# Optimization experiments

Hardware: AMD Instinct MI355X
Metric: run time of the kernel (lower is better)

The kernel has to match this reference:

```python
import jax, jax.numpy as jnp
import numpy as np

EOS = 1  # EOS_VALUE in the original code (word_label == 1 triggers end_sentence)
L_LAYERS = 2
B, T, H, E = 128, 256, 1024, 1024  # TD == E == input_size


def setup_inputs() -> dict:
    key = jax.random.key(0)
    ks = jax.random.split(key, 20)
    k = 1.0 / np.sqrt(H)
    u = lambda kk, shape: jax.random.uniform(kk, shape, jnp.float32, -k, k)
    inp = {
        "yy_pad": jax.random.randint(ks[0], (B, T), 0, E, dtype=jnp.int32),
        "h_t": jax.random.normal(ks[1], (L_LAYERS, B, H), jnp.float32),
        "h_t_rev": jax.random.normal(ks[2], (L_LAYERS, B, H), jnp.float32),
        "x_lens": jax.random.randint(ks[3], (B,), 1, T - 1, dtype=jnp.int32).at[0].set(T - 1),
        # parameters (layer 0 input size == E == H, so weights stack cleanly)
        "emb": jax.random.normal(ks[4], (E, E), jnp.float32) * 0.02,
        "W_ih": u(ks[5], (L_LAYERS, 4 * H, E)),
        "W_hh": u(ks[6], (L_LAYERS, 4 * H, H)),
        "b_ih": u(ks[7], (L_LAYERS, 4 * H)),
        "b_hh": u(ks[8], (L_LAYERS, 4 * H)),
        "W_ih_rev": u(ks[9], (L_LAYERS, 4 * H, E)),
        "W_hh_rev": u(ks[10], (L_LAYERS, 4 * H, H)),
        "b_ih_rev": u(ks[11], (L_LAYERS, 4 * H)),
        "b_hh_rev": u(ks[12], (L_LAYERS, 4 * H)),
        "c0": jnp.zeros((L_LAYERS, H), jnp.float32),
        "c0_rev": jnp.zeros((L_LAYERS, H), jnp.float32),
        "fc_W": u(ks[13], (E, 2 * H)),
        "fc_b": u(ks[14], (E,)),
    }
    return inp


def _lstm_cell(x, h, c, Wih, Whh, bih, bhh):
    # torch.nn.LSTMCell gate order: input, forget, cell(g), output
    z = x @ Wih.T + bih + h @ Whh.T + bhh  # [B, 4H]
    i, f, g, o = jnp.split(z, 4, axis=-1)
    c2 = jax.nn.sigmoid(f) * c + jax.nn.sigmoid(i) * jnp.tanh(g)
    h2 = jax.nn.sigmoid(o) * jnp.tanh(c2)
    return h2, c2


def reference(yy_pad, h_t, h_t_rev, x_lens, emb, W_ih, W_hh, b_ih, b_hh,
              W_ih_rev, W_hh_rev, b_ih_rev, b_hh_rev, c0, c0_rev, fc_W, fc_b):
    batch = yy_pad.shape[0]
    n_steps = yy_pad.shape[1]  # == max(x_lens) + 1 by construction (static)
    eos_onehot = jax.nn.one_hot(EOS, fc_W.shape[0], dtype=fc_W.dtype)  # [TD]

    c_init = jnp.broadcast_to(c0[:, None, :], (L_LAYERS, batch, c0.shape[1]))
    c_init_rev = jnp.broadcast_to(c0_rev[:, None, :], (L_LAYERS, batch, c0.shape[1]))

    def step(carry, _):
        feed, h, hr, c, cr, ended = carry
        x = emb[feed]   # [B, E]  (sos embedding / previous argmax token)
        xr = x
        hs, hrs, cs, crs = [], [], [], []
        for l in range(L_LAYERS):
            hn, cn = _lstm_cell(x, h[l], c[l], W_ih[l], W_hh[l], b_ih[l], b_hh[l])
            hrn, crn = _lstm_cell(xr, hr[l], cr[l], W_ih_rev[l], W_hh_rev[l], b_ih_rev[l], b_hh_rev[l])
            hs.append(hn); cs.append(cn); hrs.append(hrn); crs.append(crn)
            x, xr = hn, hrn
        h, hr = jnp.stack(hs), jnp.stack(hrs)
        c, cr = jnp.stack(cs), jnp.stack(crs)
        # faithful to torch: cat([B,H],[B,H]) -> [B,2H] -> permute(1,0) -> reshape(B,-1)
        wh = jnp.concatenate([h[-1], hr[-1]], axis=-1).T.reshape(batch, -1)
        logits = wh @ fc_W.T + fc_b  # [B, TD]
        logits = jnp.where(ended[:, None], eos_onehot, logits)
        label = jnp.argmax(logits, axis=1).astype(jnp.int32)
        ended = ended | (label == EOS)
        return (label, h, hr, c, cr, ended), logits

    carry0 = (yy_pad[:, 0], h_t, h_t_rev, c_init, c_init_rev,
              jnp.zeros((batch,), jnp.bool_))
    _, logits_seq = jax.lax.scan(step, carry0, None, length=n_steps)  # [T, B, TD]
    return jax.nn.softmax(jnp.transpose(logits_seq, (1, 0, 2)), axis=-1)  # [B, T, TD]
```

## Files before the change

kernel.cpp:

```cpp
#include <hip/hip_runtime.h>
#include <math.h>

#define NB 128
#define NT 256
#define NH 1024
#define NE 1024
#define G4 4096
#define EOSL 1

#define Z_OFF    ((size_t)0)
#define C_OFF    ((size_t)1048576)
#define HT_OFF   ((size_t)1572864)
#define FCZ_OFF  ((size_t)1835008)
#define BIAS_OFF ((size_t)2883584)
#define END_OFF  ((size_t)2899968)
#define XPH_OFF  ((size_t)2900096)
#define XPX_OFF  ((size_t)3424384)
#define WP_OFF   ((size_t)3555456)
#define TOTAL_MIN_F  ((size_t)3555456)
#define TOTAL_PACK_F ((size_t)37109888)

typedef __attribute__((ext_vector_type(8))) short s8v;
typedef __attribute__((ext_vector_type(4))) float f4v;

struct GMF {
  const float* W[16];
  const unsigned short* Bp[16];
  const unsigned short* Wp[2];
};

__device__ __forceinline__ void add4(float4& d, const float4 a) {
  d.x += a.x; d.y += a.y; d.z += a.z; d.w += a.w;
}
__device__ __forceinline__ float sigmoid_stable(float x) {
  if (x >= 0.f) return 1.f / (1.f + expf(-x));
  float ex = expf(x);
  return ex / (1.f + ex);
}
__device__ __forceinline__ unsigned short bf_rne(float x) {
  unsigned u = __float_as_uint(x);
  return (unsigned short)((u + 0x7FFFu + ((u >> 16) & 1u)) >> 16);
}
__device__ __forceinline__ void split_bf(float x, unsigned short& h, unsigned short& l) {
  unsigned u = __float_as_uint(x);
  unsigned hb = (u + 0x7FFFu + ((u >> 16) & 1u)) >> 16;
  h = (unsigned short)hb;
  float r = x - __uint_as_float(hb << 16);
  l = bf_rne(r);
}
__device__ __forceinline__ void cvt8(float4 a0, float4 a1, s8v& hi, s8v& lo)
{
  const float v[8] = {a0.x, a0.y, a0.z, a0.w, a1.x, a1.y, a1.z, a1.w};
  #pragma unroll
  for (int j = 0; j < 8; j++) {
    unsigned short h, l; split_bf(v[j], h, l);
    hi[j] = (short)h; lo[j] = (short)l;
  }
}


__global__ void k_init(const int* yy, const float* h_t, const float* h_tr,
                       const float* c0, const float* c0r,
                       const float* b_ih, const float* b_hh,
                       const float* b_ihr, const float* b_hhr,
                       const float* emb,
                       unsigned short* xph, unsigned short* xpx,
                       float* call, float* bias, int* ended)
{
  int idx = blockIdx.x * 256 + threadIdx.x;
  if (idx < 2 * 2048 * 128) {
    int dir = idx / (2048 * 128); int rem = idx % (2048 * 128);
    int row = rem >> 7, b = rem & 127;
    int l = row >> 10, n = row & 1023;
    const float* src = dir ? h_tr : h_t;
    float v = src[((size_t)l * 128 + b) * 1024 + n];
    unsigned short h, lo; split_bf(v, h, lo);
    size_t off = ((size_t)(dir * 64 + (row >> 5)) * 8 + (b >> 4)) * 1024
               + ((b & 15) + 16 * ((n >> 3) & 3)) * 8 + (n & 7);
    xph[off] = h; xph[off + 512] = lo;
  }
  if (idx < 4 * 1024 * 128) {
    int ld = idx / (1024 * 128); int l = ld >> 1, dir = ld & 1;
    int rem = idx % (1024 * 128); int n = rem >> 7;
    call[idx] = (dir ? c0r : c0)[l * 1024 + n];
  }
  if (idx < 4 * 4096) {
    int ld = idx / 4096; int l = ld >> 1, dir = ld & 1;
    int m = idx & 4095;
    bias[idx] = (dir ? b_ihr : b_ih)[l * 4096 + m] + (dir ? b_hhr : b_hh)[l * 4096 + m];
  }
  if (idx < 128 * 1024) {
    int b = idx >> 10, k = idx & 1023;
    int e = yy[b * NT];
    float v = emb[(size_t)e * 1024 + k];
    unsigned short h, lo; split_bf(v, h, lo);
    size_t off = ((size_t)(k >> 5) * 8 + (b >> 4)) * 1024
               + ((b & 15) + 16 * ((k >> 3) & 3)) * 8 + (k & 7);
    xpx[off] = h; xpx[off + 512] = lo;
  }
  if (idx < NB) ended[idx] = 0;
}

__global__ void k_packW(const float* W_ih, const float* W_hh,
                        const float* W_ihr, const float* W_hhr,
                        unsigned short* WP)
{
  int idx = blockIdx.x * 256 + threadIdx.x;
  int l = idx & 63;
  int frag = idx >> 6;
  int ktile = frag & 63;
  int mtile = (frag >> 6) & 255;
  int ld = frag >> 14;
  int layer = ld >> 1, dir = ld & 1;
  int m = mtile * 16 + (l & 15);
  int kg = ktile * 32 + (l >> 4) * 8;
  const float* base;
  if (kg < 1024) base = (dir ? W_ihr : W_ih) + ((size_t)layer * 4096 + m) * 1024 + kg;
  else           base = (dir ? W_hhr : W_hh) + ((size_t)layer * 4096 + m) * 1024 + (kg - 1024);
  float4 a0 = *(const float4*)base, a1 = *(const float4*)(base + 4);
  s8v hi, lo; cvt8(a0, a1, hi, lo);
  unsigned short* outp = WP + (size_t)frag * 1024 + l * 8;
  *(s8v*)outp = hi;
  *(s8v*)(outp + 512) = lo;
}

__device__ __forceinline__ void red_write(float* red, int slot, int l, const f4v (&acc)[2][8])
{
  #pragma unroll
  for (int mt = 0; mt < 2; mt++)
    #pragma unroll
    for (int bt = 0; bt < 8; bt++)
      *(f4v*)&red[(size_t)slot * 4096 + (mt * 8 + bt) * 256 + l * 4] = acc[mt][bt];
}
__device__ __forceinline__ void red_add(const float* red, int slot, int l, f4v (&acc)[2][8])
{
  #pragma unroll
  for (int mt = 0; mt < 2; mt++)
    #pragma unroll
    for (int bt = 0; bt < 8; bt++)
      acc[mt][bt] += *(const f4v*)&red[(size_t)slot * 4096 + (mt * 8 + bt) * 256 + l * 4];
}

template<int PACKED>
__global__ __launch_bounds__(512, 2) void k_gemm(GMF d, float* z)
{
  const int mb = blockIdx.x, dir = blockIdx.y;
  const int tid = threadIdx.x, l = tid & 63, w = tid >> 6;
  const int m0 = mb * 32;
  const int lr = l & 15, lk = l >> 4;
  __shared__ __align__(16) float red[4 * 4096];

  f4v acc[2][8];
  #pragma unroll
  for (int mt = 0; mt < 2; mt++)
    #pragma unroll
    for (int bt = 0; bt < 8; bt++)
      acc[mt][bt] = (f4v)(0.0f);

  const unsigned short* Bb = d.Bp[dir * 8 + w] + l * 8;

  if (PACKED) {
    const unsigned short* Wb = d.Wp[dir]
        + (((size_t)(mb * 2) * 64 + w * 8) << 10) + l * 8;
    s8v whc[2], wlc[2];
    #pragma unroll
    for (int mt = 0; mt < 2; mt++) {
      const unsigned short* p = Wb + ((size_t)(mt * 64) << 10);
      whc[mt] = *(const s8v*)p; wlc[mt] = *(const s8v*)(p + 512);
    }
    #pragma unroll 1
    for (int kk = 0; kk < 8; kk++) {
      s8v bh[8], bl[8];
      #pragma unroll
      for (int bt = 0; bt < 8; bt++) {
        const unsigned short* p = Bb + ((size_t)(kk * 8 + bt) << 10);
        bh[bt] = *(const s8v*)p; bl[bt] = *(const s8v*)(p + 512);
      }
      s8v whn[2], wln[2];
      if (kk < 7) {
        #pragma unroll
        for (int mt = 0; mt < 2; mt++) {
          const unsigned short* p = Wb + ((size_t)(mt * 64 + kk + 1) << 10);
          whn[mt] = *(const s8v*)p; wln[mt] = *(const s8v*)(p + 512);
        }
      }
      #pragma unroll
      for (int mt = 0; mt < 2; mt++)
        #pragma unroll
        for (int bt = 0; bt < 8; bt++) {
          acc[mt][bt] = __builtin_amdgcn_mfma_f32_16x16x32_bf16(whc[mt], bh[bt], acc[mt][bt], 0, 0, 0);
          acc[mt][bt] = __builtin_amdgcn_mfma_f32_16x16x32_bf16(whc[mt], bl[bt], acc[mt][bt], 0, 0, 0);
          acc[mt][bt] = __builtin_amdgcn_mfma_f32_16x16x32_bf16(wlc[mt], bh[bt], acc[mt][bt], 0, 0, 0);
        }
      if (kk < 7) {
        whc[0] = whn[0]; whc[1] = whn[1];
        wlc[0] = wln[0]; wlc[1] = wln[1];
      }
    }
  } else {
    const float* Wb = d.W[dir * 8 + w] + (size_t)(m0 + lr) * 1024 + lk * 8;
    float4 ac[2][2];
    #pragma unroll
    for (int mt = 0; mt < 2; mt++) {
      ac[mt][0] = *(const float4*)(Wb + (size_t)mt * 16384);
      ac[mt][1] = *(const float4*)(Wb + (size_t)mt * 16384 + 4);
    }
    #pragma unroll 1
    for (int kk = 0; kk < 8; kk++) {
      s8v bh[8], bl[8];
      #pragma unroll
      for (int bt = 0; bt < 8; bt++) {
        const unsigned short* p = Bb + ((size_t)(kk * 8 + bt) << 10);
        bh[bt] = *(const s8v*)p; bl[bt] = *(const s8v*)(p + 512);
      }
      float4 an[2][2];
      if (kk < 7) {
        #pragma unroll
        for (int mt = 0; mt < 2; mt++) {
          an[mt][0] = *(const float4*)(Wb + (size_t)mt * 16384 + (kk + 1) * 32);
          an[mt][1] = *(const float4*)(Wb + (size_t)mt * 16384 + (kk + 1) * 32 + 4);
        }
      }
      #pragma unroll
      for (int mt = 0; mt < 2; mt++) {
        s8v wh, wl;
        cvt8(ac[mt][0], ac[mt][1], wh, wl);
        #pragma unroll
        for (int bt = 0; bt < 8; bt++) {
          acc[mt][bt] = __builtin_amdgcn_mfma_f32_16x16x32_bf16(wh, bh[bt], acc[mt][bt], 0, 0, 0);
          acc[mt][bt] = __builtin_amdgcn_mfma_f32_16x16x32_bf16(wh, bl[bt], acc[mt][bt], 0, 0, 0);
          acc[mt][bt] = __builtin_amdgcn_mfma_f32_16x16x32_bf16(wl, bh[bt], acc[mt][bt], 0, 0, 0);
        }
      }
      if (kk < 7) {
        #pragma unroll
        for (int mt = 0; mt < 2; mt++) { ac[mt][0] = an[mt][0]; ac[mt][1] = an[mt][1]; }
      }
    }
  }

  if (w >= 4) red_write(red, w - 4, l, acc);
  __syncthreads();
  if (w < 4) red_add(red, w, l, acc);
  __syncthreads();
  if (w == 2 || w == 3) red_write(red, w - 2, l, acc);
  __syncthreads();
  if (w < 2) red_add(red, w, l, acc);
  __syncthreads();
  if (w < 2) red_write(red, w, l, acc);
  __syncthreads();
  float* zb = z + (size_t)dir * 4096 * 128;
  #pragma unroll
  for (int vi = 0; vi < 2; vi++) {
    int v = tid + vi * 512;
    f4v s = *(const f4v*)&red[(size_t)v * 4];
    s += *(const f4v*)&red[(size_t)4096 + (size_t)v * 4];
    int frag = v >> 6, lane = v & 63;
    int mt = frag >> 3, bt = frag & 7;
    int m = m0 + mt * 16 + (lane >> 4) * 4;
    int b = bt * 16 + (lane & 15);
    #pragma unroll
    for (int r = 0; r < 4; r++)
      zb[(size_t)(m + r) * 128 + b] = s[r];
  }
}

__global__ void k_gates(const float* z, const float* bias, float* c,
                        unsigned short* xph, int ktile0, float* hB)
{
  int t = threadIdx.x;
  int idx = blockIdx.x * 256 + t;
  int n = idx >> 5, cc = (idx & 31) << 2;
  int dir = blockIdx.y;
  float4 g[4];
  #pragma unroll
  for (int gg = 0; gg < 4; gg++) {
    int row = gg * 1024 + n;
    float4 s = *(const float4*)(z + ((size_t)dir * 4096 + row) * 128 + cc);
    float b = bias[dir * 4096 + row];
    s.x += b; s.y += b; s.z += b; s.w += b;
    g[gg] = s;
  }
  float* cp = c + ((size_t)dir * 1024 + n) * 128 + cc;
  float4 cold = *(float4*)cp;
  float4 cn, hn;
  cn.x = sigmoid_stable(g[1].x) * cold.x + sigmoid_stable(g[0].x) * tanhf(g[2].x);
  cn.y = sigmoid_stable(g[1].y) * cold.y + sigmoid_stable(g[0].y) * tanhf(g[2].y);
  cn.z = sigmoid_stable(g[1].z) * cold.z + sigmoid_stable(g[0].z) * tanhf(g[2].z);
  cn.w = sigmoid_stable(g[1].w) * cold.w + sigmoid_stable(g[0].w) * tanhf(g[2].w);
  hn.x = sigmoid_stable(g[3].x) * tanhf(cn.x);
  hn.y = sigmoid_stable(g[3].y) * tanhf(cn.y);
  hn.z = sigmoid_stable(g[3].z) * tanhf(cn.z);
  hn.w = sigmoid_stable(g[3].w) * tanhf(cn.w);
  *(float4*)cp = cn;
  size_t fo = ((size_t)(dir * 64 + ktile0 + (n >> 5)) * 8 + (cc >> 4)) * 1024
            + ((cc & 15) + 16 * ((n >> 3) & 3)) * 8 + (n & 7);
  const float* hv = &hn.x;
  #pragma unroll
  for (int j = 0; j < 4; j++) {
    unsigned short h, lo; split_bf(hv[j], h, lo);
    xph[fo + j * 8] = h;
    xph[fo + j * 8 + 512] = lo;
  }
  if (hB)
    *(float4*)(hB + (size_t)dir * (1024 * 128) + (size_t)n * 128 + cc) = hn;
}

__global__ __launch_bounds__(256) void k_fc(const float* Ht, const float* fc_W, float* fcz)
{
  int et = blockIdx.x, kp = blockIdx.y;
  int e0 = et * 64;
  int k00 = kp * 256;
  __shared__ __align__(16) float in_s[128][36];
  __shared__ __align__(16) float w_s[64][36];
  int t = threadIdx.x, e_sub = t & 7, bg = t >> 3, b0 = bg * 4;
  float acc[8][4] = {};
  for (int kc = 0; kc < 256; kc += 32) {
    #pragma unroll
    for (int i = 0; i < 4; i++) {
      int flat = t + 256 * i, r = flat >> 3, f4i = flat & 7;
      const float* row = Ht + (r >= 64 ? (size_t)NH * NB + (size_t)(r - 64) * 2048
                                       : (size_t)r * 2048);
      float4 v = *(const float4*)(row + k00 + kc + f4i * 4);
      int sw = (f4i ^ (r >> 2)) & 7;
      *(float4*)&in_s[r][sw * 4] = v;
    }
    #pragma unroll
    for (int i = 0; i < 2; i++) {
      int flat = t + 256 * i, r = flat >> 3, f4i = flat & 7;
      *(float4*)&w_s[r][f4i * 4] =
          *(const float4*)(fc_W + (size_t)(e0 + r) * 2048 + k00 + kc + f4i * 4);
    }
    __syncthreads();
    #pragma unroll
    for (int kq = 0; kq < 8; kq++) {
      int ksw = (kq ^ bg) & 7;
      float4 a4[4];
      #pragma unroll
      for (int ib = 0; ib < 4; ib++) a4[ib] = *(const float4*)&in_s[b0 + ib][ksw * 4];
      float4 w4[8];
      #pragma unroll
      for (int je = 0; je < 8; je++) w4[je] = *(const float4*)&w_s[e_sub + 8 * je][kq * 4];
      #pragma unroll
      for (int je = 0; je < 8; je++)
        #pragma unroll
        for (int ib = 0; ib < 4; ib++)
          acc[je][ib] += a4[ib].x * w4[je].x + a4[ib].y * w4[je].y +
                         a4[ib].z * w4[je].z + a4[ib].w * w4[je].w;
    }
    __syncthreads();
  }
  for (int je = 0; je < 8; je++) {
    int e = e0 + e_sub + 8 * je;
    for (int ib = 0; ib < 4; ib++)
      fcz[((size_t)kp * NB + b0 + ib) * NE + e] = acc[je][ib];
  }
}

__global__ void k_final(const float* fcz, const float* fc_b, int* ended,
                        float* out, int tstep, const float* emb, unsigned short* xpx)
{
  int b = blockIdx.x;
  int t = threadIdx.x;
  __shared__ float sval[256];
  __shared__ int   sidx[256];
  __shared__ float ssum[256];
  bool end = (ended[b] != 0);
  float v[4];
  int e_base = t * 4;
  float4 vv = *(const float4*)&fc_b[e_base];
  #pragma unroll
  for (int p = 0; p < 8; p++)
    add4(vv, *(const float4*)&fcz[((size_t)p * NB + b) * NE + e_base]);
  v[0] = vv.x; v[1] = vv.y; v[2] = vv.z; v[3] = vv.w;
  if (end) {
    #pragma unroll
    for (int j = 0; j < 4; j++) v[j] = (e_base + j == EOSL) ? 1.f : 0.f;
  }
  float bv = v[0]; int bi = e_base;
  #pragma unroll
  for (int j = 1; j < 4; j++) if (v[j] > bv) { bv = v[j]; bi = e_base + j; }
  sval[t] = bv; sidx[t] = bi;
  __syncthreads();
  for (int s = 128; s > 0; s >>= 1) {
    if (t < s) {
      float ov = sval[t + s]; int oi = sidx[t + s];
      if (ov > sval[t] || (ov == sval[t] && oi < sidx[t])) { sval[t] = ov; sidx[t] = oi; }
    }
    __syncthreads();
  }
  float m = sval[0]; int label = sidx[0];
  {
    int k0 = t * 4;
    float4 e4 = *(const float4*)(emb + (size_t)label * 1024 + k0);
    size_t off = ((size_t)(k0 >> 5) * 8 + (b >> 4)) * 1024
               + ((b & 15) + 16 * ((k0 >> 3) & 3)) * 8 + (k0 & 7);
    ushort4 h4, l4;
    unsigned short hh, ll;
    split_bf(e4.x, hh, ll); h4.x = hh; l4.x = ll;
    split_bf(e4.y, hh, ll); h4.y = hh; l4.y = ll;
    split_bf(e4.z, hh, ll); h4.z = hh; l4.z = ll;
    split_bf(e4.w, hh, ll); h4.w = hh; l4.w = ll;
    *(ushort4*)(xpx + off) = h4;
    *(ushort4*)(xpx + off + 512) = l4;
  }
  float ls = 0.f;
  #pragma unroll
  for (int j = 0; j < 4; j++) { v[j] = expf(v[j] - m); ls += v[j]; }
  ssum[t] = ls;
  __syncthreads();
  for (int s = 128; s > 0; s >>= 1) { if (t < s) ssum[t] += ssum[t + s]; __syncthreads(); }
  float inv = 1.f / ssum[0];
  float* orow = out + ((size_t)b * NT + tstep) * NE + e_base;
  #pragma unroll
  for (int j = 0; j < 4; j++) orow[j] = v[j] * inv;
  if (t == 0) ended[b] = (end || label == EOSL) ? 1 : 0;
}

extern "C" void kernel_launch(void* const* d_in, const int* in_sizes, int n_in,
                              void* d_out, int out_size, void* d_ws, size_t ws_size,
                              hipStream_t stream)
{
  const int*   yy    = (const int*)d_in[0];
  const float* h_t   = (const float*)d_in[1];
  const float* h_tr  = (const float*)d_in[2];
  const float* emb   = (const float*)d_in[4];
  const float* W_ih  = (const float*)d_in[5];
  const float* W_hh  = (const float*)d_in[6];
  const float* b_ih  = (const float*)d_in[7];
  const float* b_hh  = (const float*)d_in[8];
  const float* W_ihr = (const float*)d_in[9];
  const float* W_hhr = (const float*)d_in[10];
  const float* b_ihr = (const float*)d_in[11];
  const float* b_hhr = (const float*)d_in[12];
  const float* c0    = (const float*)d_in[13];
  const float* c0r   = (const float*)d_in[14];
  const float* fc_W  = (const float*)d_in[15];
  const float* fc_b  = (const float*)d_in[16];
  float* out = (float*)d_out;

  float* ws   = (float*)d_ws;
  float* z    = ws + Z_OFF;
  float* call = ws + C_OFF;
  float* Ht   = ws + HT_OFF;
  float* fcz  = ws + FCZ_OFF;
  float* bias = ws + BIAS_OFF;
  int* ended  = (int*)(ws + END_OFF);
  unsigned short* xph = (unsigned short*)(ws + XPH_OFF);
  unsigned short* xpx = (unsigned short*)(ws + XPX_OFF);
  unsigned short* WP  = (unsigned short*)(ws + WP_OFF);
  bool packed = ws_size >= TOTAL_PACK_F * sizeof(float);

  k_init<<<2048, 256, 0, stream>>>(yy, h_t, h_tr, c0, c0r, b_ih, b_hh, b_ihr, b_hhr,
                                   emb, xph, xpx, call, bias, ended);
  if (packed)
    k_packW<<<16384, 256, 0, stream>>>(W_ih, W_hh, W_ihr, W_hhr, WP);

  GMF d0, d1;
  for (int dir = 0; dir < 2; dir++) {
    const float* Wih0 = dir ? W_ihr : W_ih;
    const float* Whh0 = dir ? W_hhr : W_hh;
    const float* Wih1 = Wih0 + (size_t)G4 * NH;
    const float* Whh1 = Whh0 + (size_t)G4 * NH;
    for (int ks = 0; ks < 8; ks++) {
      d0.W[dir * 8 + ks]  = (ks < 4) ? (Wih0 + ks * 256) : (Whh0 + (ks - 4) * 256);
      d0.Bp[dir * 8 + ks] = (ks < 4) ? (xpx + (size_t)(ks * 64) * 1024)
                                     : (xph + (size_t)((dir * 64 + (ks - 4) * 8) * 8) * 1024);
      d1.W[dir * 8 + ks]  = (ks < 4) ? (Wih1 + ks * 256) : (Whh1 + (ks - 4) * 256);
      d1.Bp[dir * 8 + ks] = xph + (size_t)((dir * 64 + ks * 8) * 8) * 1024;
    }
    d0.Wp[dir] = WP + (size_t)(0 * 2 + dir) * 256 * 64 * 1024;
    d1.Wp[dir] = WP + (size_t)(1 * 2 + dir) * 256 * 64 * 1024;
  }

  for (int t = 0; t < NT; t++) {
    if (packed) k_gemm<1><<<dim3(128, 2), 512, 0, stream>>>(d0, z);
    else        k_gemm<0><<<dim3(128, 2), 512, 0, stream>>>(d0, z);
    k_gates<<<dim3(128, 2), 256, 0, stream>>>(z, bias, call, xph, 0, nullptr);
    if (packed) k_gemm<1><<<dim3(128, 2), 512, 0, stream>>>(d1, z);
    else        k_gemm<0><<<dim3(128, 2), 512, 0, stream>>>(d1, z);
    k_gates<<<dim3(128, 2), 256, 0, stream>>>(z, bias + 2 * 4096,
                                              call + (size_t)2 * 1024 * 128, xph, 32, Ht);
    k_fc<<<dim3(16, 8), 256, 0, stream>>>(Ht, fc_W, fcz);
    k_final<<<128, 256, 0, stream>>>(fcz, fc_b, ended, out, t, emb, xpx);
  }
}
```

Before: 23.95 ms.

## Fuse LSTM gate computation into GEMM kernel with gate-interleaved weight rows

Weight packing is reordered so each 32-row block holds all four gates (i,f,g,o) for the same 8 hidden units. The GEMM epilogue can then apply the LSTM cell update directly from LDS. The separate gates kernel and the z workspace round-trip are removed, and h is double-buffered across timesteps so in-place writes cannot race with reads. Per step this cuts launches from six to four and removes global traffic for z, at the cost of a heavier epilogue in which only 256 of the 512 threads do cell math.

```diff
diff --git a/kernel.cpp b/kernel.cpp
--- a/kernel.cpp
+++ b/kernel.cpp
@@ -8,34 +8,28 @@
 #define G4 4096
 #define EOSL 1
 
-#define Z_OFF    ((size_t)0)
-#define C_OFF    ((size_t)1048576)
-#define HT_OFF   ((size_t)1572864)
-#define FCZ_OFF  ((size_t)1835008)
-#define BIAS_OFF ((size_t)2883584)
-#define END_OFF  ((size_t)2899968)
-#define XPH_OFF  ((size_t)2900096)
-#define XPX_OFF  ((size_t)3424384)
-#define WP_OFF   ((size_t)3555456)
-#define TOTAL_MIN_F  ((size_t)3555456)
-#define TOTAL_PACK_F ((size_t)37109888)
+#define C_OFF    ((size_t)0)
+#define HT_OFF   ((size_t)524288)
+#define FCZ_OFF  ((size_t)786432)
+#define BIAS_OFF ((size_t)1835008)
+#define END_OFF  ((size_t)1851392)
+#define XPH_OFF  ((size_t)1851520)
+#define XPX_OFF  ((size_t)2900096)
+#define WP_OFF   ((size_t)3031168)
+#define TOTAL_MIN_F  ((size_t)3031168)
+#define TOTAL_PACK_F ((size_t)36585600)
 
 typedef __attribute__((ext_vector_type(8))) short s8v;
 typedef __attribute__((ext_vector_type(4))) float f4v;
-
-struct GMF {
-  const float* W[16];
-  const unsigned short* Bp[16];
-  const unsigned short* Wp[2];
-};
-
-__device__ __forceinline__ void add4(float4& d, const float4 a) {
-  d.x += a.x; d.y += a.y; d.z += a.z; d.w += a.w;
-}
+typedef __attribute__((ext_vector_type(2))) unsigned u2v;
+
 __device__ __forceinline__ float sigmoid_stable(float x) {
   if (x >= 0.f) return 1.f / (1.f + expf(-x));
   float ex = expf(x);
   return ex / (1.f + ex);
+}
+__device__ __forceinline__ void add4(float4& d, const float4 a) {
+  d.x += a.x; d.y += a.y; d.z += a.z; d.w += a.w;
 }
 __device__ __forceinline__ unsigned short bf_rne(float x) {
   unsigned u = __float_as_uint(x);
@@ -80,9 +74,11 @@
     xph[off] = h; xph[off + 512] = lo;
   }
   if (idx < 4 * 1024 * 128) {
-    int ld = idx / (1024 * 128); int l = ld >> 1, dir = ld & 1;
-    int rem = idx % (1024 * 128); int n = rem >> 7;
-    call[idx] = (dir ? c0r : c0)[l * 1024 + n];
+    int ld = idx / (1024 * 128); int l = ld >> 1;
+    int rem = idx % (1024 * 128);
+    int mb = rem >> 10, nl = rem & 7;
+    const float* cs = (ld & 1) ? c0r : c0;
+    call[idx] = cs[l * 1024 + mb * 8 + nl];
   }
   if (idx < 4 * 4096) {
     int ld = idx / 4096; int l = ld >> 1, dir = ld & 1;
@@ -112,7 +108,10 @@
   int mtile = (frag >> 6) & 255;
   int ld = frag >> 14;
   int layer = ld >> 1, dir = ld & 1;
-  int m = mtile * 16 + (l & 15);
+  int s = l & 15;
+  int mbb = mtile >> 1, half = mtile & 1;
+  int gate = half * 2 + (s >> 3);
+  int m = gate * 1024 + mbb * 8 + (s & 7);
   int kg = ktile * 32 + (l >> 4) * 8;
   const float* base;
   if (kg < 1024) base = (dir ? W_ihr : W_ih) + ((size_t)layer * 4096 + m) * 1024 + kg;
@@ -140,50 +139,40 @@
     for (int bt = 0; bt < 8; bt++)
       acc[mt][bt] += *(const f4v*)&red[(size_t)slot * 4096 + (mt * 8 + bt) * 256 + l * 4];
 }
+__device__ __forceinline__ void gloadW(const unsigned short* Wb, int kk,
+                                       s8v (&h)[2], s8v (&lo)[2])
+{
+  #pragma unroll
+  for (int mt = 0; mt < 2; mt++) {
+    const unsigned short* q = Wb + ((size_t)(mt * 64 + kk) << 10);
+    h[mt] = *(const s8v*)q; lo[mt] = *(const s8v*)(q + 512);
+  }
+}
+__device__ __forceinline__ void gloadB(const unsigned short* Bb, int kk,
+                                       s8v (&h)[8], s8v (&lo)[8])
+{
+  #pragma unroll
+  for (int bt = 0; bt < 8; bt++) {
+    const unsigned short* q = Bb + ((size_t)(kk * 8 + bt) << 10);
+    h[bt] = *(const s8v*)q; lo[bt] = *(const s8v*)(q + 512);
+  }
+}
 
 template<int PACKED>
-__global__ __launch_bounds__(512, 2) void k_gemm(GMF d, float* z)
-{
-  const int mb = blockIdx.x, dir = blockIdx.y;
-  const int tid = threadIdx.x, l = tid & 63, w = tid >> 6;
-  const int m0 = mb * 32;
-  const int lr = l & 15, lk = l >> 4;
-  __shared__ __align__(16) float red[4 * 4096];
-
-  f4v acc[2][8];
-  #pragma unroll
-  for (int mt = 0; mt < 2; mt++)
-    #pragma unroll
-    for (int bt = 0; bt < 8; bt++)
-      acc[mt][bt] = (f4v)(0.0f);
-
-  const unsigned short* Bb = d.Bp[dir * 8 + w] + l * 8;
-
+__device__ __forceinline__ void gemm_k256(f4v (&acc)[2][8],
+                                          const unsigned short* Wb,
+                                          const float* Wrow0, const float* Wrow1,
+                                          const unsigned short* Bb)
+{
   if (PACKED) {
-    const unsigned short* Wb = d.Wp[dir]
-        + (((size_t)(mb * 2) * 64 + w * 8) << 10) + l * 8;
     s8v whc[2], wlc[2];
-    #pragma unroll
-    for (int mt = 0; mt < 2; mt++) {
-      const unsigned short* p = Wb + ((size_t)(mt * 64) << 10);
-      whc[mt] = *(const s8v*)p; wlc[mt] = *(const s8v*)(p + 512);
-    }
+    gloadW(Wb, 0, whc, wlc);
     #pragma unroll 1
     for (int kk = 0; kk < 8; kk++) {
       s8v bh[8], bl[8];
-      #pragma unroll
-      for (int bt = 0; bt < 8; bt++) {
-        const unsigned short* p = Bb + ((size_t)(kk * 8 + bt) << 10);
-        bh[bt] = *(const s8v*)p; bl[bt] = *(const s8v*)(p + 512);
-      }
+      gloadB(Bb, kk, bh, bl);
       s8v whn[2], wln[2];
-      if (kk < 7) {
-        #pragma unroll
-        for (int mt = 0; mt < 2; mt++) {
-          const unsigned short* p = Wb + ((size_t)(mt * 64 + kk + 1) << 10);
-          whn[mt] = *(const s8v*)p; wln[mt] = *(const s8v*)(p + 512);
-        }
-      }
+      if (kk < 7) gloadW(Wb, kk + 1, whn, wln);
       #pragma unroll
       for (int mt = 0; mt < 2; mt++)
         #pragma unroll
@@ -198,27 +187,23 @@
       }
     }
   } else {
-    const float* Wb = d.W[dir * 8 + w] + (size_t)(m0 + lr) * 1024 + lk * 8;
+    const float* Wrow[2] = { Wrow0, Wrow1 };
     float4 ac[2][2];
     #pragma unroll
     for (int mt = 0; mt < 2; mt++) {
-      ac[mt][0] = *(const float4*)(Wb + (size_t)mt * 16384);
-      ac[mt][1] = *(const float4*)(Wb + (size_t)mt * 16384 + 4);
+      ac[mt][0] = *(const float4*)(Wrow[mt]);
+      ac[mt][1] = *(const float4*)(Wrow[mt] + 4);
     }
     #pragma unroll 1
     for (int kk = 0; kk < 8; kk++) {
       s8v bh[8], bl[8];
-      #pragma unroll
-      for (int bt = 0; bt < 8; bt++) {
-        const unsigned short* p = Bb + ((size_t)(kk * 8 + bt) << 10);
-        bh[bt] = *(const s8v*)p; bl[bt] = *(const s8v*)(p + 512);
-      }
+      gloadB(Bb, kk, bh, bl);
       float4 an[2][2];
       if (kk < 7) {
         #pragma unroll
         for (int mt = 0; mt < 2; mt++) {
-          an[mt][0] = *(const float4*)(Wb + (size_t)mt * 16384 + (kk + 1) * 32);
-          an[mt][1] = *(const float4*)(Wb + (size_t)mt * 16384 + (kk + 1) * 32 + 4);
+          an[mt][0] = *(const float4*)(Wrow[mt] + (kk + 1) * 32);
+          an[mt][1] = *(const float4*)(Wrow[mt] + (kk + 1) * 32 + 4);
         }
       }
       #pragma unroll
@@ -238,72 +223,126 @@
       }
     }
   }
-
-  if (w >= 4) red_write(red, w - 4, l, acc);
-  __syncthreads();
-  if (w < 4) red_add(red, w, l, acc);
-  __syncthreads();
-  if (w == 2 || w == 3) red_write(red, w - 2, l, acc);
-  __syncthreads();
-  if (w < 2) red_add(red, w, l, acc);
-  __syncthreads();
-  if (w < 2) red_write(red, w, l, acc);
-  __syncthreads();
-  float* zb = z + (size_t)dir * 4096 * 128;
+}
+
+__device__ __forceinline__ void reduce_to_zs(float* lds, int tid, int l, int w,
+                                             f4v (&acc)[2][8])
+{
+  if (w >= 4) red_write(lds, w - 4, l, acc);
+  __syncthreads();
+  if (w < 4) red_add(lds, w, l, acc);
+  __syncthreads();
+  if (w == 2 || w == 3) red_write(lds, w - 2, l, acc);
+  __syncthreads();
+  if (w < 2) red_add(lds, w, l, acc);
+  __syncthreads();
+  if (w < 2) red_write(lds, w, l, acc);
+  __syncthreads();
+  float* zs = lds + 8192;
   #pragma unroll
   for (int vi = 0; vi < 2; vi++) {
     int v = tid + vi * 512;
-    f4v s = *(const f4v*)&red[(size_t)v * 4];
-    s += *(const f4v*)&red[(size_t)4096 + (size_t)v * 4];
+    f4v s = *(const f4v*)&lds[(size_t)v * 4];
+    s += *(const f4v*)&lds[4096 + (size_t)v * 4];
     int frag = v >> 6, lane = v & 63;
     int mt = frag >> 3, bt = frag & 7;
-    int m = m0 + mt * 16 + (lane >> 4) * 4;
-    int b = bt * 16 + (lane & 15);
+    int s0 = (lane >> 4) * 4, bcol = bt * 16 + (lane & 15);
     #pragma unroll
     for (int r = 0; r < 4; r++)
-      zb[(size_t)(m + r) * 128 + b] = s[r];
-  }
-}
-
-__global__ void k_gates(const float* z, const float* bias, float* c,
-                        unsigned short* xph, int ktile0, float* hB)
-{
-  int t = threadIdx.x;
-  int idx = blockIdx.x * 256 + t;
-  int n = idx >> 5, cc = (idx & 31) << 2;
-  int dir = blockIdx.y;
-  float4 g[4];
-  #pragma unroll
-  for (int gg = 0; gg < 4; gg++) {
-    int row = gg * 1024 + n;
-    float4 s = *(const float4*)(z + ((size_t)dir * 4096 + row) * 128 + cc);
-    float b = bias[dir * 4096 + row];
-    s.x += b; s.y += b; s.z += b; s.w += b;
-    g[gg] = s;
-  }
-  float* cp = c + ((size_t)dir * 1024 + n) * 128 + cc;
-  float4 cold = *(float4*)cp;
-  float4 cn, hn;
-  cn.x = sigmoid_stable(g[1].x) * cold.x + sigmoid_stable(g[0].x) * tanhf(g[2].x);
-  cn.y = sigmoid_stable(g[1].y) * cold.y + sigmoid_stable(g[0].y) * tanhf(g[2].y);
-  cn.z = sigmoid_stable(g[1].z) * cold.z + sigmoid_stable(g[0].z) * tanhf(g[2].z);
-  cn.w = sigmoid_stable(g[1].w) * cold.w + sigmoid_stable(g[0].w) * tanhf(g[2].w);
-  hn.x = sigmoid_stable(g[3].x) * tanhf(cn.x);
-  hn.y = sigmoid_stable(g[3].y) * tanhf(cn.y);
-  hn.z = sigmoid_stable(g[3].z) * tanhf(cn.z);
-  hn.w = sigmoid_stable(g[3].w) * tanhf(cn.w);
-  *(float4*)cp = cn;
-  size_t fo = ((size_t)(dir * 64 + ktile0 + (n >> 5)) * 8 + (cc >> 4)) * 1024
-            + ((cc & 15) + 16 * ((n >> 3) & 3)) * 8 + (n & 7);
-  const float* hv = &hn.x;
-  #pragma unroll
-  for (int j = 0; j < 4; j++) {
-    unsigned short h, lo; split_bf(hv[j], h, lo);
-    xph[fo + j * 8] = h;
-    xph[fo + j * 8 + 512] = lo;
-  }
-  if (hB)
-    *(float4*)(hB + (size_t)dir * (1024 * 128) + (size_t)n * 128 + cc) = hn;
+      zs[mt * 2048 + (s0 + r) * 128 + bcol] = s[r];
+  }
+  __syncthreads();
+}
+
+struct CellP {
+  const unsigned short* WP;
+  const float* Wih; const float* Whh; const float* Wihr; const float* Whhr;
+  const float* bias; float* c; const unsigned short* xpx; float* Ht;
+};
+
+template<int LAYER, int PACKED>
+__global__ __launch_bounds__(512, 2) void k_cell(CellP p, const unsigned short* xpR,
+                                                 unsigned short* xpW)
+{
+  __shared__ __align__(16) float lds[16384];
+  const int mb = blockIdx.x, dir = blockIdx.y, tid = threadIdx.x;
+  const int l = tid & 63, w = tid >> 6;
+  const int lr = l & 15, lk = l >> 4;
+
+  const unsigned short* Bb;
+  if (LAYER == 0)
+    Bb = (w < 4) ? p.xpx + (size_t)w * 65536
+                 : xpR + (size_t)(dir * 64 + (w - 4) * 8) * 8192;
+  else
+    Bb = (w < 4) ? xpW + (size_t)(dir * 64 + w * 8) * 8192
+                 : xpR + (size_t)(dir * 64 + 32 + (w - 4) * 8) * 8192;
+  Bb += l * 8;
+
+  f4v acc[2][8];
+  #pragma unroll
+  for (int mt = 0; mt < 2; mt++)
+    #pragma unroll
+    for (int bt = 0; bt < 8; bt++)
+      acc[mt][bt] = (f4v)(0.0f);
+
+  if (PACKED) {
+    const unsigned short* Wb = p.WP + (size_t)(LAYER * 2 + dir) * 16777216ULL
+        + (((size_t)(mb * 2) * 64 + (size_t)w * 8) << 10) + l * 8;
+    gemm_k256<1>(acc, Wb, nullptr, nullptr, Bb);
+  } else {
+    const float* Wsel = ((w < 4) ? (dir ? p.Wihr : p.Wih) : (dir ? p.Whhr : p.Whh))
+                      + (size_t)LAYER * 4194304;
+    int col0 = (w & 3) * 256 + lk * 8;
+    const float* Wr0 = Wsel + ((size_t)(((lr >> 3)) * 1024 + mb * 8 + (lr & 7))) * 1024 + col0;
+    const float* Wr1 = Wsel + ((size_t)((2 + (lr >> 3)) * 1024 + mb * 8 + (lr & 7))) * 1024 + col0;
+    gemm_k256<0>(acc, nullptr, Wr0, Wr1, Bb);
+  }
+
+  reduce_to_zs(lds, tid, l, w, acc);
+  float* zs = lds + 8192;
+
+  int ldg = LAYER * 2 + dir;
+  if (tid < 256) {
+    int b = tid & 127, q = tid >> 7;
+    float* cp = p.c + ((((size_t)ldg * 128 + mb) * 128 + b) * 8 + q * 4);
+    f4v cold = *(const f4v*)cp;
+    f4v cnew;
+    float hs[4];
+    #pragma unroll
+    for (int j = 0; j < 4; j++) {
+      int nl = q * 4 + j;
+      int n = mb * 8 + nl;
+      float iv = zs[nl * 128 + b]              + p.bias[ldg * 4096 + n];
+      float fv = zs[(nl + 8) * 128 + b]        + p.bias[ldg * 4096 + 1024 + n];
+      float gv = zs[2048 + nl * 128 + b]       + p.bias[ldg * 4096 + 2048 + n];
+      float ov = zs[2048 + (nl + 8) * 128 + b] + p.bias[ldg * 4096 + 3072 + n];
+      float co = cold[j];
+      float cn = sigmoid_stable(fv) * co + sigmoid_stable(iv) * tanhf(gv);
+      float hn = sigmoid_stable(ov) * tanhf(cn);
+      cnew[j] = cn;
+      hs[j] = hn;
+    }
+    *(f4v*)cp = cnew;
+    unsigned short hh[4], ll[4];
+    #pragma unroll
+    for (int j = 0; j < 4; j++) split_bf(hs[j], hh[j], ll[j]);
+    int kt = LAYER * 32 + (mb >> 2);
+    size_t off = ((size_t)(dir * 64 + kt) * 8 + (b >> 4)) * 1024
+               + ((size_t)((b & 15) + 16 * (mb & 3))) * 8 + q * 4;
+    u2v vh; vh.x = (unsigned)hh[0] | ((unsigned)hh[1] << 16);
+            vh.y = (unsigned)hh[2] | ((unsigned)hh[3] << 16);
+    u2v vl; vl.x = (unsigned)ll[0] | ((unsigned)ll[1] << 16);
+            vl.y = (unsigned)ll[2] | ((unsigned)ll[3] << 16);
+    *(u2v*)(xpW + off) = vh;
+    *(u2v*)(xpW + off + 512) = vl;
+    if (LAYER == 1) {
+      #pragma unroll
+      for (int j = 0; j < 4; j++) {
+        int n = mb * 8 + q * 4 + j;
+        p.Ht[(size_t)dir * 131072 + (size_t)n * 128 + b] = hs[j];
+      }
+    }
+  }
 }
 
 __global__ __launch_bounds__(256) void k_fc(const float* Ht, const float* fc_W, float* fcz)
@@ -439,8 +478,7 @@
   const float* fc_b  = (const float*)d_in[16];
   float* out = (float*)d_out;
 
-  float* ws   = (float*)d_ws;
-  float* z    = ws + Z_OFF;
+  float* ws = (float*)d_ws;
   float* call = ws + C_OFF;
   float* Ht   = ws + HT_OFF;
   float* fcz  = ws + FCZ_OFF;
@@ -456,31 +494,21 @@
   if (packed)
     k_packW<<<16384, 256, 0, stream>>>(W_ih, W_hh, W_ihr, W_hhr, WP);
 
-  GMF d0, d1;
-  for (int dir = 0; dir < 2; dir++) {
-    const float* Wih0 = dir ? W_ihr : W_ih;
-    const float* Whh0 = dir ? W_hhr : W_hh;
-    const float* Wih1 = Wih0 + (size_t)G4 * NH;
-    const float* Whh1 = Whh0 + (size_t)G4 * NH;
-    for (int ks = 0; ks < 8; ks++) {
-      d0.W[dir * 8 + ks]  = (ks < 4) ? (Wih0 + ks * 256) : (Whh0 + (ks - 4) * 256);
-      d0.Bp[dir * 8 + ks] = (ks < 4) ? (xpx + (size_t)(ks * 64) * 1024)
-                                     : (xph + (size_t)((dir * 64 + (ks - 4) * 8) * 8) * 1024);
-      d1.W[dir * 8 + ks]  = (ks < 4) ? (Wih1 + ks * 256) : (Whh1 + (ks - 4) * 256);
-      d1.Bp[dir * 8 + ks] = xph + (size_t)((dir * 64 + ks * 8) * 8) * 1024;
-    }
-    d0.Wp[dir] = WP + (size_t)(0 * 2 + dir) * 256 * 64 * 1024;
-    d1.Wp[dir] = WP + (size_t)(1 * 2 + dir) * 256 * 64 * 1024;
-  }
+  CellP cp;
+  cp.WP = WP;
+  cp.Wih = W_ih; cp.Whh = W_hh; cp.Wihr = W_ihr; cp.Whhr = W_hhr;
+  cp.bias = bias; cp.c = call; cp.xpx = xpx; cp.Ht = Ht;
 
   for (int t = 0; t < NT; t++) {
-    if (packed) k_gemm<1><<<dim3(128, 2), 512, 0, stream>>>(d0, z);
-    else        k_gemm<0><<<dim3(128, 2), 512, 0, stream>>>(d0, z);
-    k_gates<<<dim3(128, 2), 256, 0, stream>>>(z, bias, call, xph, 0, nullptr);
-    if (packed) k_gemm<1><<<dim3(128, 2), 512, 0, stream>>>(d1, z);
-    else        k_gemm<0><<<dim3(128, 2), 512, 0, stream>>>(d1, z);
-    k_gates<<<dim3(128, 2), 256, 0, stream>>>(z, bias + 2 * 4096,
-                                              call + (size_t)2 * 1024 * 128, xph, 32, Ht);
+    const unsigned short* xpR = xph + (size_t)(t & 1) * 1048576;
+    unsigned short* xpW = xph + (size_t)((t & 1) ^ 1) * 1048576;
+    if (packed) {
+      k_cell<0, 1><<<dim3(128, 2), 512, 0, stream>>>(cp, xpR, xpW);
+      k_cell<1, 1><<<dim3(128, 2), 512, 0, stream>>>(cp, xpR, xpW);
+    } else {
+      k_cell<0, 0><<<dim3(128, 2), 512, 0, stream>>>(cp, xpR, xpW);
+      k_cell<1, 0><<<dim3(128, 2), 512, 0, stream>>>(cp, xpR, xpW);
+    }
     k_fc<<<dim3(16, 8), 256, 0, stream>>>(Ht, fc_W, fcz);
     k_final<<<128, 256, 0, stream>>>(fcz, fc_b, ended, out, t, emb, xpx);
   }
```

After: 22.78 ms. 1.05x faster.
